# Kernel tuning notes

Hardware: AMD Instinct MI355X
Metric: run time of the kernel (lower is better)

The kernel has to match this reference:

```python
import jax, jax.numpy as jnp
import numpy as np

N_SPECIAL = 4
LABEL_ID = 3
C_ACT = 64
C_TIME = 32
ACT_START = N_SPECIAL
TIME_START = N_SPECIAL + C_ACT
VOCAB = TIME_START + C_TIME  # 100
B, T, D = 8, 2048, 256


def l2norm(x, eps=1e-12):
    n = jnp.sqrt(jnp.sum(x * x, axis=-1, keepdims=True))
    return x / jnp.maximum(n, eps)


def causal_proto(h_norm, is_label, nxt, lo, hi, E_cls, alpha):
    """At every <LABEL> position L, build per-class prototypes from earlier
    support label positions (class = next token at that position), add a
    Bayesian prior alpha*E_cls, and return cosine sims of h_norm[L] vs protos.
    Non-label positions (or labels with no earlier support) -> zeros.
    Implemented as a single causal scan over time (online running sums)."""
    Bv, Tv, Dv = h_norm.shape
    C = E_cls.shape[0]
    is_sup = is_label & (nxt >= lo) & (nxt < hi)          # [B,T]
    cls = jnp.clip(nxt - lo, 0, C - 1)                    # [B,T]

    def step(carry, xs):
        Hsum, cnt = carry                                  # [B,C,D], [B,C]
        h_t, cls_t, sup_t, lab_t = xs                      # [B,D],[B],[B],[B]
        proto = l2norm((Hsum + alpha * E_cls) / (cnt[:, :, None] + alpha + 1e-8))
        sims = jnp.einsum('bd,bcd->bc', h_t, proto)        # cosine (h_t is unit)
        valid = lab_t & (jnp.sum(cnt, axis=-1) > 0)        # any earlier support
        out = jnp.where(valid[:, None], sims, 0.0)
        oh = jax.nn.one_hot(cls_t, C, dtype=h_t.dtype) * sup_t[:, None].astype(h_t.dtype)
        Hsum = Hsum + oh[:, :, None] * h_t[:, None, :]
        cnt = cnt + oh
        return (Hsum, cnt), out

    init = (jnp.zeros((Bv, C, Dv), h_norm.dtype), jnp.zeros((Bv, C), h_norm.dtype))
    xs = (jnp.swapaxes(h_norm, 0, 1), jnp.swapaxes(cls, 0, 1),
          jnp.swapaxes(is_sup, 0, 1), jnp.swapaxes(is_label, 0, 1))
    _, outs = jax.lax.scan(jax.checkpoint(step), init, xs)
    return jnp.swapaxes(outs, 0, 1)                        # [B,T,C]


def setup_inputs() -> dict:
    key = jax.random.key(0)
    ks = jax.random.split(key, 6)
    f32 = jnp.float32
    return {
        'tokens': jax.random.randint(ks[0], (B, T), 0, VOCAB, dtype=jnp.int32),
        'h': jax.random.normal(ks[1], (B, T, D), dtype=f32),
        'E': jax.random.normal(ks[2], (VOCAB, D), dtype=f32) * 0.02,
        'W_next': jax.random.normal(ks[3], (C_ACT, D), dtype=f32) * 0.02,
        'b_next': jnp.zeros((C_ACT,), f32),
        'W_time': jax.random.normal(ks[4], (C_TIME, D), dtype=f32) * 0.02,
        'b_time': jnp.zeros((C_TIME,), f32),
        'tied_scale_act': jnp.array(0.0, f32),
        'tied_scale_time': jnp.array(0.0, f32),
        'proto_scale_act': jnp.array(1.0, f32),
        'proto_scale_time': jnp.array(1.0, f32),
        'proto_prior_act': jnp.array(0.5, f32),
        'proto_prior_time': jnp.array(0.5, f32),
        'proto_temp_act': jnp.array(1.0, f32),
        'proto_temp_time': jnp.array(1.0, f32),
    }


def reference(tokens, h, E, W_next, b_next, W_time, b_time,
              tied_scale_act, tied_scale_time, proto_scale_act, proto_scale_time,
              proto_prior_act, proto_prior_time, proto_temp_act, proto_temp_time):
    sp = jax.nn.softplus
    # parametric heads
    param_next = jnp.einsum('btd,cd->btc', h, W_next) + b_next
    param_time = jnp.einsum('btd,cd->btc', h, W_time) + b_time
    # weight-tied heads (gradient flows into E here)
    tied_act = jnp.einsum('btd,cd->btc', h, E[ACT_START:TIME_START])
    tied_time = jnp.einsum('btd,cd->btc', h, E[TIME_START:VOCAB])
    # prototype head (E detached, as in the torch code)
    h_norm = l2norm(h)
    E_det = jax.lax.stop_gradient(E)
    E_act = l2norm(E_det[ACT_START:TIME_START])
    E_time = l2norm(E_det[TIME_START:VOCAB])
    nxt = jnp.roll(tokens, -1, axis=1)
    is_label = tokens == LABEL_ID
    proto_act = causal_proto(h_norm, is_label, nxt, ACT_START, TIME_START,
                             E_act, sp(proto_prior_act)) * sp(proto_temp_act)
    proto_time = causal_proto(h_norm, is_label, nxt, TIME_START, VOCAB,
                              E_time, sp(proto_prior_time)) * sp(proto_temp_time)
    activity_logits = param_next + sp(tied_scale_act) * tied_act + sp(proto_scale_act) * proto_act
    time_logits = param_time + sp(tied_scale_time) * tied_time + sp(proto_scale_time) * proto_time
    return (activity_logits, time_logits)
```

## Files before the change

### kernel.cpp

```cpp
#include <hip/hip_runtime.h>
#include <hip/hip_bf16.h>

#define Bv 8
#define Tv 2048
#define Dv 256
#define C_ACT 64
#define C_TIME 32
#define NCLS 96
#define LABEL_ID 3
#define ACT_START 4
#define TIME_START 68
#define VOCAB 100
#define MAXEV 36

typedef short bf16x8 __attribute__((ext_vector_type(8)));
typedef float f32x4  __attribute__((ext_vector_type(4)));
typedef unsigned short u16x8 __attribute__((ext_vector_type(8)));

__device__ __forceinline__ float bf2f(__hip_bfloat16 x) { return __bfloat162float(x); }
__device__ __forceinline__ float bfb(unsigned short u) {
    union { unsigned int i; float f; } x; x.i = ((unsigned int)u) << 16; return x.f;
}
__device__ __forceinline__ short f2bs(float x) {
    __hip_bfloat16 b = __float2bfloat16(x);
    return *reinterpret_cast<short*>(&b);
}
__device__ __forceinline__ float spf(float x) { return log1pf(expf(x)); }

__device__ __forceinline__ float ldx(const void* p, size_t i, bool f32) {
    return f32 ? ((const float*)p)[i] : bf2f(((const __hip_bfloat16*)p)[i]);
}
__device__ __forceinline__ void stx(void* p, size_t i, float v, bool f32) {
    if (f32) ((float*)p)[i] = v;
    else     ((__hip_bfloat16*)p)[i] = __float2bfloat16(v);
}
__device__ __forceinline__ float4 ld4(const void* p, size_t i, bool f32) {
    if (f32) return *reinterpret_cast<const float4*>((const float*)p + i);
    ushort4 s = *reinterpret_cast<const ushort4*>((const unsigned short*)p + i);
    float4 u; u.x = bfb(s.x); u.y = bfb(s.y); u.z = bfb(s.z); u.w = bfb(s.w);
    return u;
}

__device__ __forceinline__ bool detect_f32_256(const void* h, int tid, int* s_cnt)
{
    if (tid == 0) *s_cnt = 0;
    __syncthreads();
    ushort4 u = *(reinterpret_cast<const ushort4*>(h) + tid);
    int c = 0; float v;
    v = bfb(u.x); if (!(fabsf(v) < 1e20f)) c++;
    v = bfb(u.y); if (!(fabsf(v) < 1e20f)) c++;
    v = bfb(u.z); if (!(fabsf(v) < 1e20f)) c++;
    v = bfb(u.w); if (!(fabsf(v) < 1e20f)) c++;
    #pragma unroll
    for (int o = 32; o > 0; o >>= 1) c += __shfl_down(c, o);
    if ((tid & 63) == 0 && c) atomicAdd(s_cnt, c);
    __syncthreads();
    return *s_cnt >= 4;
}

__device__ __forceinline__ size_t out_idx(int b, int L, int c)
{
    return (c < C_ACT)
        ? ((size_t)(b * Tv + L) * C_ACT + c)
        : ((size_t)Bv * Tv * C_ACT + (size_t)(b * Tv + L) * C_TIME + (c - C_ACT));
}

#define K1_ROWS 64
#define EVLD 264
#define GLD 44

__global__ __launch_bounds__(256) void k_all(
    const int* __restrict__ tokens,
    const void* __restrict__ h,
    const void* __restrict__ E,
    const void* __restrict__ Wn, const void* __restrict__ bn,
    const void* __restrict__ Wt, const void* __restrict__ bt,
    const void* ts_a, const void* ts_t,
    const void* ps_a, const void* ps_t,
    const void* pp_a, const void* pp_t,
    const void* pt_a, const void* pt_t,
    void* __restrict__ out)
{
    __shared__ union {
        unsigned short mB[NCLS][EVLD];
        struct {
            unsigned short hb[48][EVLD];
            union {
                unsigned short AsMs[48][EVLD];
                struct {
                    float Gl[MAXEV][GLD];
                    float P[MAXEV][24];
                    float Pm[MAXEV][24];
                    float SG[MAXEV][24];
                    float ZP[MAXEV][24];
                } r;
            } u2;
            float nrm[MAXEV];
        } s;
    } u;
    __shared__ int s_pos[MAXEV], s_cls[MAXEV];
    __shared__ unsigned long long s_mask[32];
    __shared__ unsigned long long s_mact, s_mtim;
    __shared__ int s_cnt, s_evn;

    int tid = threadIdx.x;
    bool f32 = detect_f32_256(h, tid, &s_cnt);
    float spt_a = spf(ldx(ts_a, 0, f32));
    float spt_t = spf(ldx(ts_t, 0, f32));

    if (blockIdx.x >= 32) {
        int R0   = (blockIdx.x - 32) * K1_ROWS;
        int w    = tid >> 6;
        int lane = tid & 63;
        int lr   = lane & 15;
        int quad = lane >> 4;

        int rowb = 16 * w + quad * 4;
        int tk[4]; float bs[6];
        #pragma unroll
        for (int r = 0; r < 4; ++r) tk[r] = tokens[R0 + rowb + r];
        #pragma unroll
        for (int n = 0; n < 6; ++n) {
            int c = 16 * n + lr;
            bs[n] = (c < C_ACT) ? ldx(bn, c, f32) : ldx(bt, c - C_ACT, f32);
        }

        #pragma unroll 4
        for (int k = 0; k < 12; ++k) {
            int f = tid + 256 * k;
            int c = f >> 5, col = (f & 31) * 8;
            bool act = c < C_ACT;
            size_t wrow = act ? (size_t)c : (size_t)(c - C_ACT);
            size_t erow = act ? (size_t)(ACT_START + c) : (size_t)(TIME_START + (c - C_ACT));
            const void* wptr = act ? Wn : Wt;
            float spt = act ? spt_a : spt_t;
            float4 w0 = ld4(wptr, wrow * Dv + col,     f32);
            float4 w1 = ld4(wptr, wrow * Dv + col + 4, f32);
            float4 e0 = ld4(E,    erow * Dv + col,     f32);
            float4 e1 = ld4(E,    erow * Dv + col + 4, f32);
            u16x8 m8;
            m8[0] = (unsigned short)f2bs(w0.x + spt * e0.x);
            m8[1] = (unsigned short)f2bs(w0.y + spt * e0.y);
            m8[2] = (unsigned short)f2bs(w0.z + spt * e0.z);
            m8[3] = (unsigned short)f2bs(w0.w + spt * e0.w);
            m8[4] = (unsigned short)f2bs(w1.x + spt * e1.x);
            m8[5] = (unsigned short)f2bs(w1.y + spt * e1.y);
            m8[6] = (unsigned short)f2bs(w1.z + spt * e1.z);
            m8[7] = (unsigned short)f2bs(w1.w + spt * e1.w);
            *reinterpret_cast<u16x8*>(&u.mB[c][col]) = m8;
        }

        bf16x8 av[8];
        if (!f32) {
            const unsigned short* aB = (const unsigned short*)h
                + (size_t)(R0 + 16 * w + lr) * Dv + quad * 8;
            #pragma unroll
            for (int dc = 0; dc < 4; ++dc)
                #pragma unroll
                for (int ks = 0; ks < 2; ++ks)
                    av[dc * 2 + ks] = *reinterpret_cast<const bf16x8*>(
                        aB + dc * 64 + ks * 32);
        } else {
            const float* aB = (const float*)h
                + (size_t)(R0 + 16 * w + lr) * Dv + quad * 8;
            #pragma unroll
            for (int dc = 0; dc < 4; ++dc)
                #pragma unroll
                for (int ks = 0; ks < 2; ++ks) {
                    float4 a0 = *reinterpret_cast<const float4*>(aB + dc * 64 + ks * 32);
                    float4 a1 = *reinterpret_cast<const float4*>(aB + dc * 64 + ks * 32 + 4);
                    bf16x8 a;
                    a[0] = f2bs(a0.x); a[1] = f2bs(a0.y); a[2] = f2bs(a0.z); a[3] = f2bs(a0.w);
                    a[4] = f2bs(a1.x); a[5] = f2bs(a1.y); a[6] = f2bs(a1.z); a[7] = f2bs(a1.w);
                    av[dc * 2 + ks] = a;
                }
        }

        __syncthreads();

        f32x4 acc[6];
        #pragma unroll
        for (int n = 0; n < 6; ++n) acc[n] = (f32x4){0.f, 0.f, 0.f, 0.f};
        #pragma unroll
        for (int dc = 0; dc < 4; ++dc) {
            #pragma unroll
            for (int ks = 0; ks < 2; ++ks) {
                bf16x8 a = av[dc * 2 + ks];
                int koff = dc * 64 + ks * 32 + quad * 8;
                #pragma unroll
                for (int n = 0; n < 6; ++n) {
                    bf16x8 b = *reinterpret_cast<const bf16x8*>(
                        &u.mB[16 * n + lr][koff]);
                    acc[n] = __builtin_amdgcn_mfma_f32_16x16x32_bf16(a, b, acc[n], 0, 0, 0);
                }
            }
        }

        #pragma unroll
        for (int n = 0; n < 6; ++n) {
            int c = 16 * n + lr;
            #pragma unroll
            for (int r = 0; r < 4; ++r) {
                if (tk[r] == LABEL_ID) continue;
                int row = R0 + rowb + r;
                stx(out, out_idx(row >> 11, row & (Tv - 1), c), acc[n][r] + bs[n], f32);
            }
        }
        return;
    }

    int b  = blockIdx.x >> 2;
    int q  = blockIdx.x & 3;
    int c0 = q * 24;
    int lane = tid & 63, wvx = tid >> 6;

    int* s_tok = reinterpret_cast<int*>(&u.s.u2.AsMs[0][0]);
    #pragma unroll
    for (int k = 0; k < 8; ++k) {
        int i = tid + 256 * k;
        int tok = tokens[(size_t)b * Tv + i];
        s_tok[i] = tok;
        unsigned long long m = __ballot(tok == LABEL_ID);
        if (lane == 0) s_mask[wvx + 4 * k] = m;
    }
    __syncthreads();

    if (wvx == 0) {
        unsigned long long m = (lane < 32) ? s_mask[lane] : 0ull;
        int cnt = __popcll(m);
        int x = cnt;
        #pragma unroll
        for (int d = 1; d < 32; d <<= 1) {
            int src = lane - d;
            int y = __shfl(x, src < 0 ? 0 : src);
            if (lane >= d) x += y;
        }
        if (lane < 32) {
            int n = x - cnt;
            unsigned long long mm = m;
            while (mm && n < MAXEV) {
                int bit = __builtin_ctzll(mm);
                s_pos[n++] = lane * 64 + bit;
                mm &= mm - 1;
            }
        }
        if (lane == 31) s_evn = (x < MAXEV) ? x : MAXEV;
    }
    __syncthreads();
    int evn = s_evn;
    int nrt = (evn + 15) >> 4;

    if (tid < evn) {
        int nxt = s_tok[(s_pos[tid] + 1) & (Tv - 1)];
        int c = -1;
        if (nxt >= ACT_START && nxt < TIME_START)  c = nxt - ACT_START;
        else if (nxt >= TIME_START && nxt < VOCAB) c = C_ACT + (nxt - TIME_START);
        s_cls[tid] = c;
    }

    {
        float4 hv[9];
        #pragma unroll
        for (int k = 0; k < 9; ++k) {
            int i = wvx + 4 * k;
            if (i < evn)
                hv[k] = ld4(h, ((size_t)b * Tv + s_pos[i]) * Dv + lane * 4, f32);
        }
        #pragma unroll
        for (int k = 0; k < 9; ++k) {
            int i = wvx + 4 * k;
            if (i < evn) {
                float4 v = hv[k];
                float p = v.x * v.x + v.y * v.y + v.z * v.z + v.w * v.w;
                #pragma unroll
                for (int o = 32; o > 0; o >>= 1) p += __shfl_xor(p, o);
                float nr = fmaxf(sqrtf(p), 1e-12f);
                float inv = 1.0f / nr;
                ushort4 s4;
                s4.x = (unsigned short)f2bs(v.x * inv);
                s4.y = (unsigned short)f2bs(v.y * inv);
                s4.z = (unsigned short)f2bs(v.z * inv);
                s4.w = (unsigned short)f2bs(v.w * inv);
                *reinterpret_cast<ushort4*>(&u.s.hb[i][lane * 4]) = s4;
                if (lane == 0) u.s.nrm[i] = nr;
            }
        }
        for (int i = evn + wvx; i < 16 * nrt; i += 4) {
            ushort4 z; z.x = z.y = z.z = z.w = 0;
            *reinterpret_cast<ushort4*>(&u.s.hb[i][lane * 4]) = z;
        }
    }
    __syncthreads();

    float alpha_a = spf(ldx(pp_a, 0, f32));
    float alpha_t = spf(ldx(pp_t, 0, f32));

    {
        float4 ev[6], wv6[6];
        #pragma unroll
        for (int k = 0; k < 6; ++k) {
            int lc = wvx + 4 * k, c = c0 + lc;
            bool act = c < C_ACT;
            int erow = act ? (ACT_START + c) : (TIME_START + (c - C_ACT));
            size_t wrow = act ? (size_t)c : (size_t)(c - C_ACT);
            ev[k]  = ld4(E, (size_t)erow * Dv + lane * 4, f32);
            wv6[k] = ld4(act ? Wn : Wt, wrow * Dv + lane * 4, f32);
        }
        #pragma unroll
        for (int k = 0; k < 6; ++k) {
            int lc = wvx + 4 * k, c = c0 + lc;
            bool act = c < C_ACT;
            float4 e4 = ev[k], w4 = wv6[k];
            float p = e4.x * e4.x + e4.y * e4.y + e4.z * e4.z + e4.w * e4.w;
            #pragma unroll
            for (int o = 32; o > 0; o >>= 1) p += __shfl_xor(p, o);
            float alpha = act ? alpha_a : alpha_t;
            float ai  = alpha / fmaxf(sqrtf(p), 1e-12f);
            float spt = act ? spt_a : spt_t;
            ushort4 a4, m4;
            a4.x = (unsigned short)f2bs(e4.x * ai);
            a4.y = (unsigned short)f2bs(e4.y * ai);
            a4.z = (unsigned short)f2bs(e4.z * ai);
            a4.w = (unsigned short)f2bs(e4.w * ai);
            m4.x = (unsigned short)f2bs(w4.x + spt * e4.x);
            m4.y = (unsigned short)f2bs(w4.y + spt * e4.y);
            m4.z = (unsigned short)f2bs(w4.z + spt * e4.z);
            m4.w = (unsigned short)f2bs(w4.w + spt * e4.w);
            *reinterpret_cast<ushort4*>(&u.s.u2.AsMs[lc][lane * 4])      = a4;
            *reinterpret_cast<ushort4*>(&u.s.u2.AsMs[24 + lc][lane * 4]) = m4;
        }
    }
    __syncthreads();

    {
        int lr2 = lane & 15, quad2 = lane >> 4;
        int nct = 3 + nrt;
        int TT  = nrt * nct;
        f32x4 accs[5];
        #pragma unroll
        for (int kk = 0; kk < 5; ++kk) {
            int t = wvx + 4 * kk;
            if (t < TT) {
                int rt2 = t / nct, ct = t - rt2 * nct;
                int ar = 16 * rt2 + lr2;
                const unsigned short* bbase = (ct < 3)
                    ? &u.s.u2.AsMs[16 * ct + lr2][0]
                    : &u.s.hb[16 * (ct - 3) + lr2][0];
                f32x4 acc = (f32x4){0.f, 0.f, 0.f, 0.f};
                #pragma unroll
                for (int ks = 0; ks < 8; ++ks) {
                    bf16x8 a  = *reinterpret_cast<const bf16x8*>(
                        &u.s.hb[ar][ks * 32 + quad2 * 8]);
                    bf16x8 bf = *reinterpret_cast<const bf16x8*>(
                        &bbase[ks * 32 + quad2 * 8]);
                    acc = __builtin_amdgcn_mfma_f32_16x16x32_bf16(a, bf, acc, 0, 0, 0);
                }
                accs[kk] = acc;
            }
        }
        __syncthreads();
        #pragma unroll
        for (int kk = 0; kk < 5; ++kk) {
            int t = wvx + 4 * kk;
            if (t < TT) {
                int rt2 = t / nct, ct = t - rt2 * nct;
                #pragma unroll
                for (int r = 0; r < 4; ++r) {
                    int row = 16 * rt2 + quad2 * 4 + r;
                    if (row >= evn) continue;
                    if (ct < 3) {
                        int cc = 16 * ct + lr2;
                        if (cc < 24) u.s.u2.r.P[row][cc] = accs[kk][r];
                        else         u.s.u2.r.Pm[row][cc - 24] = accs[kk][r];
                    } else {
                        int j = 16 * (ct - 3) + lr2;
                        if (j < evn) u.s.u2.r.Gl[row][j] = accs[kk][r];
                    }
                }
            }
        }
    }
    __syncthreads();

    for (int t = tid; t < evn * 24; t += 256) {
        int i = t / 24, lc = t - i * 24;
        int c = c0 + lc;
        float s = 0.f;
        #pragma unroll 4
        for (int j = 0; j < i; ++j)
            s += (s_cls[j] == c) ? u.s.u2.r.Gl[i][j] : 0.f;
        u.s.u2.r.SG[i][lc] = s;
    }
    if (wvx == 1) {
        int cj = (lane < evn) ? s_cls[lane] : -1;
        unsigned long long ma = __ballot(cj >= 0 && cj < C_ACT);
        unsigned long long mt = __ballot(cj >= C_ACT);
        if (lane == 0) { s_mact = ma; s_mtim = mt; }
    }
    __syncthreads();

    {
        int j = lane;
        float gjj = 0.f; int cj = -1;
        if (j < evn) { gjj = u.s.u2.r.Gl[j][j]; cj = s_cls[j]; }
        #pragma unroll
        for (int t6 = 0; t6 < 6; ++t6) {
            int lc = wvx * 6 + t6;
            int c = c0 + lc;
            float z = 0.f;
            if (j < evn && cj == c)
                z = 2.f * (u.s.u2.r.P[j][lc] + u.s.u2.r.SG[j][lc]) + gjj;
            float x = z;
            #pragma unroll
            for (int d = 1; d < 64; d <<= 1) {
                int src = lane - d;
                float y = __shfl(x, src < 0 ? 0 : src);
                if (lane >= d) x += y;
            }
            if (j < evn) u.s.u2.r.ZP[j][lc] = x - z;
        }
    }
    __syncthreads();

    {
        float mult_a = spf(ldx(ps_a, 0, f32)) * spf(ldx(pt_a, 0, f32));
        float mult_t = spf(ldx(ps_t, 0, f32)) * spf(ldx(pt_t, 0, f32));
        unsigned long long ma = s_mact, mt = s_mtim;
        for (int t = tid; t < evn * 24; t += 256) {
            int i = t / 24, lc = t - i * 24;
            int c = c0 + lc;
            bool actc = c < C_ACT;
            float alpha = actc ? alpha_a : alpha_t;
            float bias  = actc ? ldx(bn, c, f32) : ldx(bt, c - C_ACT, f32);
            float mult  = actc ? mult_a : mult_t;
            unsigned long long m = actc ? ma : mt;
            bool any = (m & ((1ull << i) - 1ull)) != 0ull;
            float v = u.s.u2.r.Pm[i][lc] * u.s.nrm[i] + bias;
            if (any) {
                float num = u.s.u2.r.P[i][lc] + u.s.u2.r.SG[i][lc];
                float n2  = alpha * alpha + u.s.u2.r.ZP[i][lc];
                v += mult * (num / fmaxf(sqrtf(n2), 1e-20f));
            }
            stx(out, out_idx(b, s_pos[i], c), v, f32);
        }
    }
}

extern "C" void kernel_launch(void* const* d_in, const int* in_sizes, int n_in,
                              void* d_out, int out_size, void* d_ws, size_t ws_size,
                              hipStream_t stream)
{
    const int* tokens = (const int*)d_in[0];
    const void* h    = d_in[1];
    const void* E    = d_in[2];
    const void* Wn   = d_in[3];
    const void* bn   = d_in[4];
    const void* Wt   = d_in[5];
    const void* bt   = d_in[6];
    const void* ts_a = d_in[7];
    const void* ts_t = d_in[8];
    const void* ps_a = d_in[9];
    const void* ps_t = d_in[10];
    const void* pp_a = d_in[11];
    const void* pp_t = d_in[12];
    const void* pt_a = d_in[13];
    const void* pt_t = d_in[14];

    k_all<<<32 + (Bv * Tv) / K1_ROWS, 256, 0, stream>>>(
        tokens, h, E, Wn, bn, Wt, bt,
        ts_a, ts_t, ps_a, ps_t, pp_a, pp_t, pt_a, pt_t, d_out);
}
```

Baseline: 115.1 us.

## Halve dense rows per block, hoist prototype loads, use class bitmasks for SG sums

The dense-head blocks now cover 32 rows instead of 64, with waves split two by two over row tiles and class groups, so there are more blocks and less work per wave. In the prototype blocks, the global loads of E and W are issued before the token scan so their latency overlaps it. The per-class bitmasks of earlier events are built once with ballots, and the SG prefix sum loops only over set bits instead of testing every earlier event. The risk is that twice as many dense blocks each rebuild the full 96x256 combined weight tile in shared memory, and the hoisted loads keep more registers live.

```diff
diff --git a/kernel.cpp b/kernel.cpp
--- a/kernel.cpp
+++ b/kernel.cpp
@@ -65,7 +65,7 @@
         : ((size_t)Bv * Tv * C_ACT + (size_t)(b * Tv + L) * C_TIME + (c - C_ACT));
 }
 
-#define K1_ROWS 64
+#define K1_ROWS 32
 #define EVLD 264
 #define GLD 44
 
@@ -100,6 +100,7 @@
     } u;
     __shared__ int s_pos[MAXEV], s_cls[MAXEV];
     __shared__ unsigned long long s_mask[32];
+    __shared__ unsigned long long s_bm[24];
     __shared__ unsigned long long s_mact, s_mtim;
     __shared__ int s_cnt, s_evn;
 
@@ -114,15 +115,17 @@
         int lane = tid & 63;
         int lr   = lane & 15;
         int quad = lane >> 4;
-
-        int rowb = 16 * w + quad * 4;
-        int tk[4]; float bs[6];
+        int rt   = w & 1;
+        int cg   = w >> 1;
+
+        int rowb = 16 * rt + quad * 4;
+        int tk[4]; float bs[3];
         #pragma unroll
         for (int r = 0; r < 4; ++r) tk[r] = tokens[R0 + rowb + r];
         #pragma unroll
-        for (int n = 0; n < 6; ++n) {
-            int c = 16 * n + lr;
-            bs[n] = (c < C_ACT) ? ldx(bn, c, f32) : ldx(bt, c - C_ACT, f32);
+        for (int nn = 0; nn < 3; ++nn) {
+            int c = 16 * (3 * cg + nn) + lr;
+            bs[nn] = (c < C_ACT) ? ldx(bn, c, f32) : ldx(bt, c - C_ACT, f32);
         }
 
         #pragma unroll 4
@@ -153,57 +156,48 @@
         bf16x8 av[8];
         if (!f32) {
             const unsigned short* aB = (const unsigned short*)h
-                + (size_t)(R0 + 16 * w + lr) * Dv + quad * 8;
-            #pragma unroll
-            for (int dc = 0; dc < 4; ++dc)
-                #pragma unroll
-                for (int ks = 0; ks < 2; ++ks)
-                    av[dc * 2 + ks] = *reinterpret_cast<const bf16x8*>(
-                        aB + dc * 64 + ks * 32);
+                + (size_t)(R0 + 16 * rt + lr) * Dv + quad * 8;
+            #pragma unroll
+            for (int t = 0; t < 8; ++t)
+                av[t] = *reinterpret_cast<const bf16x8*>(aB + t * 32);
         } else {
             const float* aB = (const float*)h
-                + (size_t)(R0 + 16 * w + lr) * Dv + quad * 8;
-            #pragma unroll
-            for (int dc = 0; dc < 4; ++dc)
-                #pragma unroll
-                for (int ks = 0; ks < 2; ++ks) {
-                    float4 a0 = *reinterpret_cast<const float4*>(aB + dc * 64 + ks * 32);
-                    float4 a1 = *reinterpret_cast<const float4*>(aB + dc * 64 + ks * 32 + 4);
-                    bf16x8 a;
-                    a[0] = f2bs(a0.x); a[1] = f2bs(a0.y); a[2] = f2bs(a0.z); a[3] = f2bs(a0.w);
-                    a[4] = f2bs(a1.x); a[5] = f2bs(a1.y); a[6] = f2bs(a1.z); a[7] = f2bs(a1.w);
-                    av[dc * 2 + ks] = a;
-                }
+                + (size_t)(R0 + 16 * rt + lr) * Dv + quad * 8;
+            #pragma unroll
+            for (int t = 0; t < 8; ++t) {
+                float4 a0 = *reinterpret_cast<const float4*>(aB + t * 32);
+                float4 a1 = *reinterpret_cast<const float4*>(aB + t * 32 + 4);
+                bf16x8 a;
+                a[0] = f2bs(a0.x); a[1] = f2bs(a0.y); a[2] = f2bs(a0.z); a[3] = f2bs(a0.w);
+                a[4] = f2bs(a1.x); a[5] = f2bs(a1.y); a[6] = f2bs(a1.z); a[7] = f2bs(a1.w);
+                av[t] = a;
+            }
         }
 
         __syncthreads();
 
-        f32x4 acc[6];
-        #pragma unroll
-        for (int n = 0; n < 6; ++n) acc[n] = (f32x4){0.f, 0.f, 0.f, 0.f};
-        #pragma unroll
-        for (int dc = 0; dc < 4; ++dc) {
-            #pragma unroll
-            for (int ks = 0; ks < 2; ++ks) {
-                bf16x8 a = av[dc * 2 + ks];
-                int koff = dc * 64 + ks * 32 + quad * 8;
-                #pragma unroll
-                for (int n = 0; n < 6; ++n) {
-                    bf16x8 b = *reinterpret_cast<const bf16x8*>(
-                        &u.mB[16 * n + lr][koff]);
-                    acc[n] = __builtin_amdgcn_mfma_f32_16x16x32_bf16(a, b, acc[n], 0, 0, 0);
-                }
-            }
-        }
-
-        #pragma unroll
-        for (int n = 0; n < 6; ++n) {
-            int c = 16 * n + lr;
+        f32x4 acc[3];
+        #pragma unroll
+        for (int n = 0; n < 3; ++n) acc[n] = (f32x4){0.f, 0.f, 0.f, 0.f};
+        #pragma unroll
+        for (int t = 0; t < 8; ++t) {
+            int koff = t * 32 + quad * 8;
+            #pragma unroll
+            for (int nn = 0; nn < 3; ++nn) {
+                bf16x8 b = *reinterpret_cast<const bf16x8*>(
+                    &u.mB[16 * (3 * cg + nn) + lr][koff]);
+                acc[nn] = __builtin_amdgcn_mfma_f32_16x16x32_bf16(av[t], b, acc[nn], 0, 0, 0);
+            }
+        }
+
+        #pragma unroll
+        for (int nn = 0; nn < 3; ++nn) {
+            int c = 16 * (3 * cg + nn) + lr;
             #pragma unroll
             for (int r = 0; r < 4; ++r) {
                 if (tk[r] == LABEL_ID) continue;
                 int row = R0 + rowb + r;
-                stx(out, out_idx(row >> 11, row & (Tv - 1), c), acc[n][r] + bs[n], f32);
+                stx(out, out_idx(row >> 11, row & (Tv - 1), c), acc[nn][r] + bs[nn], f32);
             }
         }
         return;
@@ -213,6 +207,20 @@
     int q  = blockIdx.x & 3;
     int c0 = q * 24;
     int lane = tid & 63, wvx = tid >> 6;
+
+    float alpha_a = spf(ldx(pp_a, 0, f32));
+    float alpha_t = spf(ldx(pp_t, 0, f32));
+
+    float4 ev[6], wv6[6];
+    #pragma unroll
+    for (int k = 0; k < 6; ++k) {
+        int lc = wvx + 4 * k, c = c0 + lc;
+        bool act = c < C_ACT;
+        int erow = act ? (ACT_START + c) : (TIME_START + (c - C_ACT));
+        size_t wrow = act ? (size_t)c : (size_t)(c - C_ACT);
+        ev[k]  = ld4(E, (size_t)erow * Dv + lane * 4, f32);
+        wv6[k] = ld4(act ? Wn : Wt, wrow * Dv + lane * 4, f32);
+    }
 
     int* s_tok = reinterpret_cast<int*>(&u.s.u2.AsMs[0][0]);
     #pragma unroll
@@ -292,20 +300,7 @@
     }
     __syncthreads();
 
-    float alpha_a = spf(ldx(pp_a, 0, f32));
-    float alpha_t = spf(ldx(pp_t, 0, f32));
-
     {
-        float4 ev[6], wv6[6];
-        #pragma unroll
-        for (int k = 0; k < 6; ++k) {
-            int lc = wvx + 4 * k, c = c0 + lc;
-            bool act = c < C_ACT;
-            int erow = act ? (ACT_START + c) : (TIME_START + (c - C_ACT));
-            size_t wrow = act ? (size_t)c : (size_t)(c - C_ACT);
-            ev[k]  = ld4(E, (size_t)erow * Dv + lane * 4, f32);
-            wv6[k] = ld4(act ? Wn : Wt, wrow * Dv + lane * 4, f32);
-        }
         #pragma unroll
         for (int k = 0; k < 6; ++k) {
             int lc = wvx + 4 * k, c = c0 + lc;
@@ -328,6 +323,16 @@
             m4.w = (unsigned short)f2bs(w4.w + spt * e4.w);
             *reinterpret_cast<ushort4*>(&u.s.u2.AsMs[lc][lane * 4])      = a4;
             *reinterpret_cast<ushort4*>(&u.s.u2.AsMs[24 + lc][lane * 4]) = m4;
+        }
+        if (wvx == 1) {
+            int cj = (lane < evn) ? s_cls[lane] : -1;
+            unsigned long long ma = __ballot(cj >= 0 && cj < C_ACT);
+            unsigned long long mt = __ballot(cj >= C_ACT);
+            if (lane == 0) { s_mact = ma; s_mtim = mt; }
+            for (int lc = 0; lc < 24; ++lc) {
+                unsigned long long bmv = __ballot(cj == c0 + lc);
+                if (lane == 0) s_bm[lc] = bmv;
+            }
         }
     }
     __syncthreads();
@@ -384,18 +389,14 @@
 
     for (int t = tid; t < evn * 24; t += 256) {
         int i = t / 24, lc = t - i * 24;
-        int c = c0 + lc;
+        unsigned long long m = s_bm[lc] & ((1ull << i) - 1ull);
         float s = 0.f;
-        #pragma unroll 4
-        for (int j = 0; j < i; ++j)
-            s += (s_cls[j] == c) ? u.s.u2.r.Gl[i][j] : 0.f;
+        while (m) {
+            int j = __builtin_ctzll(m);
+            s += u.s.u2.r.Gl[i][j];
+            m &= m - 1;
+        }
         u.s.u2.r.SG[i][lc] = s;
-    }
-    if (wvx == 1) {
-        int cj = (lane < evn) ? s_cls[lane] : -1;
-        unsigned long long ma = __ballot(cj >= 0 && cj < C_ACT);
-        unsigned long long mt = __ballot(cj >= C_ACT);
-        if (lane == 0) { s_mact = ma; s_mtim = mt; }
     }
     __syncthreads();
 
```

Result: faster. 110.2 us (-4.3%).
